# Optimization experiments

Measured on AMD Instinct MI355X. Metric: run time of the kernel, lower is better.

The kernel has to match this reference:

```python
import jax, jax.numpy as jnp
import numpy as np

# Static config (matches init_kwargs)
B, T_IN, H, W, C_IN = 32, 12, 64, 64, 4
T_OUT, C_OUT = 12, 4
K, S = 8, 4            # unfold kernel and stride (stride = K // 2); H%K==0 -> padding 0
DEC_K = 25             # series decomposition moving-average window
O = T_OUT * C_OUT      # number of per-output locally-connected filters
NH = (H - K) // S + 1  # 15
NW = (W - K) // S + 1  # 15
L = NH * NW            # 225 patches


def setup_inputs() -> dict:
    key = jax.random.key(0)
    k1, k2, k3 = jax.random.split(key, 3)
    x = jax.random.normal(k1, (B, T_IN, H, W, C_IN), jnp.float32)
    # torch init: weights ~ randn, biases zeros; stacked over the O = C_out*T_out loop
    w_s = jax.random.normal(k2, (O, T_IN, C_IN, K, K), jnp.float32)
    w_t = jax.random.normal(k3, (O, T_IN, C_IN, K, K), jnp.float32)
    b_s = jnp.zeros((O, K, K), jnp.float32)
    b_t = jnp.zeros((O, K, K), jnp.float32)
    return {"x": x, "w_s": w_s, "b_s": b_s, "w_t": w_t, "b_t": b_t}


def _moving_avg(x):
    # x: (B, T, N). Replicate-pad time by (DEC_K-1)//2 on each side, mean over DEC_K window.
    p = (DEC_K - 1) // 2
    xp = jnp.concatenate([jnp.repeat(x[:, :1], p, axis=1), x,
                          jnp.repeat(x[:, -1:], p, axis=1)], axis=1)
    cs = jnp.concatenate([jnp.zeros_like(xp[:, :1]), jnp.cumsum(xp, axis=1)], axis=1)
    return (cs[:, DEC_K:] - cs[:, :-DEC_K]) / DEC_K  # (B, T, N)


def _patch_idx():
    ii = (jnp.arange(NH) * S)[:, None] + jnp.arange(K)  # (NH, K)
    jj = (jnp.arange(NW) * S)[:, None] + jnp.arange(K)  # (NW, K)
    return ii, jj


def _unfold(x):
    # x: (B, Cc, H, W) -> patches (B, L, Cc, K, K), L row-major over (NH, NW) as in nn.Unfold
    ii, jj = _patch_idx()
    p = x[:, :, ii]              # (B, Cc, NH, K, W)
    p = p[:, :, :, :, jj]        # (B, Cc, NH, K, NW, K)
    p = p.transpose(0, 2, 4, 1, 3, 5)  # (B, NH, NW, Cc, K, K)
    return p.reshape(x.shape[0], L, x.shape[1], K, K)


def _fold(p):
    # p: (B, Cc, L, K, K) -> (B, Cc, H, W), summing overlapping contributions (nn.Fold)
    Bb, Cc = p.shape[0], p.shape[1]
    p = p.reshape(Bb, Cc, NH, NW, K, K).transpose(0, 1, 2, 4, 3, 5)  # (B,Cc,NH,K,NW,K)
    ii, jj = _patch_idx()
    I = ii[:, :, None, None]     # (NH, K, 1, 1)
    J = jj[None, None, :, :]     # (1, 1, NW, K)
    out = jnp.zeros((Bb, Cc, H, W), p.dtype)
    return out.at[:, :, I, J].add(p)


def reference(x, w_s, b_s, w_t, b_t):
    # (B, T, H, W, C) -> (B, T, C*H*W), decompose along time
    xf = x.transpose(0, 1, 4, 2, 3).reshape(B, T_IN, -1)
    trend = _moving_avg(xf)
    res = xf - trend
    out = jnp.zeros((B, L, O, K, K), x.dtype)
    for comp, w, b in ((res, w_s, b_s), (trend, w_t, b_t)):
        xc = comp.reshape(B, T_IN * C_IN, H, W)
        patches = _unfold(xc).reshape(B, L, T_IN, C_IN, K, K)
        # locally-connected linear: per (i,j) position, contract over (T_in, C_in) into O outputs
        out = out + jnp.einsum('bltcij,otcij->bloij', patches, w) + b
    out = out.transpose(0, 2, 1, 3, 4)            # (B, O, L, K, K)
    out = _fold(out)                              # (B, O, H, W)
    out = out.reshape(B, T_OUT, C_OUT, H, W).transpose(0, 1, 3, 4, 2)
    return out                                    # (B, T_out, H, W, C_out)
```

## Files before the change

kernel.cpp:

```cpp
#include <hip/hip_runtime.h>


typedef _Float16 h2 __attribute__((ext_vector_type(2)));
typedef _Float16 f16x8 __attribute__((ext_vector_type(8)));
typedef float f32x4 __attribute__((ext_vector_type(4)));
union F4F16 { float4 f4; f16x8 h8; };

__global__ __launch_bounds__(64) void pack_weights(const float* __restrict__ w_s,
                                                   const float* __restrict__ b_s,
                                                   const float* __restrict__ w_t,
                                                   const float* __restrict__ b_t,
                                                   float* __restrict__ PW) {
    int o = blockIdx.x;
    int s = threadIdx.x;
    float* dst = PW + (size_t)(s * 48 + o) * 64;
    float w0[4] = {0.f, 0.f, 0.f, 0.f};
    float w1[4] = {0.f, 0.f, 0.f, 0.f};
#pragma unroll
    for (int t = 0; t < 12; ++t) {
#pragma unroll
        for (int c = 0; c < 4; ++c) {
            int wi = ((o * 12 + t) * 4 + c) * 64 + s;
            float ws = w_s[wi];
            float wt = w_t[wi];
            dst[t * 4 + c] = ws;
            float d = wt - ws;
            w0[c] += d;
            w1[c] += (float)t * d;
        }
    }
#pragma unroll
    for (int c = 0; c < 4; ++c) {
        dst[48 + c] = w0[c];
        dst[52 + c] = w1[c];
    }
    dst[56] = b_s[o * 64 + s] + b_t[o * 64 + s];
#pragma unroll
    for (int k = 57; k < 64; ++k) dst[k] = 0.f;
}

__global__ __launch_bounds__(64) void pack_frags(const float* __restrict__ PW,
                                                 float4* __restrict__ PWF) {
    int blk = blockIdx.x;
    int cls = blk / 12;
    int to = blk % 12;
    int L = threadIdx.x;
    int n16 = L & 15, quad = L >> 4;
    int c = n16 >> 2, r = n16 & 3;
    int o = to * 4 + c;
    int rh = cls >> 2, rw = cls & 3;
    int s = (rh + 4 * (r >> 1)) * 8 + (rw + 4 * (r & 1));
    const float* src = PW + (size_t)(s * 48 + o) * 64;
#pragma unroll
    for (int ks = 0; ks < 2; ++ks) {
        F4F16 u;
#pragma unroll
        for (int j = 0; j < 8; ++j) {
            int k = ks * 32 + quad * 8 + j;
            u.h8[j] = (_Float16)src[k];
        }
        PWF[((size_t)blk * 2 + ks) * 64 + L] = u.f4;
    }
}

__global__ __launch_bounds__(256, 2) void dlinear_mfma(const float* __restrict__ x,
                                                       const float4* __restrict__ PWF,
                                                       float* __restrict__ out) {
    __shared__ float4 As[256 * 9];
    int tid = threadIdx.x;
    int wv = tid >> 6, L = tid & 63;
    int cls = blockIdx.x & 15;
    int bb = blockIdx.x >> 4;
    int rh = cls >> 2, rw = cls & 3;

    f16x8 bf[12][2];
#pragma unroll
    for (int to = 0; to < 12; ++to)
#pragma unroll
        for (int ks = 0; ks < 2; ++ks) {
            F4F16 u;
            u.f4 = PWF[((size_t)(cls * 12 + to) * 2 + ks) * 64 + L];
            bf[to][ks] = u.h8;
        }

    int hh = tid >> 4, ww = tid & 15;
    int h = 4 * hh + rh, wcol0 = 4 * ww + rw;
    const float4* xb = (const float4*)x + (size_t)bb * 12 * 4096 + h * 64 + wcol0;

    h2 X2[32] __attribute__((aligned(16)));
    {
        float sx = 0.f, sy = 0.f, sz = 0.f, sw = 0.f;
        float4 first, last;
#pragma unroll
        for (int t = 0; t < 12; ++t) {
            float4 v = xb[t * 4096];
            if (t == 0) first = v;
            if (t == 11) last = v;
            h2 a, b;
            a[0] = (_Float16)v.x; a[1] = (_Float16)v.y;
            b[0] = (_Float16)v.z; b[1] = (_Float16)v.w;
            X2[2 * t] = a;
            X2[2 * t + 1] = b;
            sx += v.x; sy += v.y; sz += v.z; sw += v.w;
        }
        const float inv25 = 1.f / 25.f;
        float A0 = (sx + 12.f * first.x + last.x) * inv25;
        float A1 = (sy + 12.f * first.y + last.y) * inv25;
        float A2 = (sz + 12.f * first.z + last.z) * inv25;
        float A3 = (sw + 12.f * first.w + last.w) * inv25;
        float D0 = (last.x - first.x) * inv25;
        float D1 = (last.y - first.y) * inv25;
        float D2 = (last.z - first.z) * inv25;
        float D3 = (last.w - first.w) * inv25;
        h2 t0, t1, t2, t3, t4, z;
        t0[0] = (_Float16)A0; t0[1] = (_Float16)A1;
        t1[0] = (_Float16)A2; t1[1] = (_Float16)A3;
        t2[0] = (_Float16)D0; t2[1] = (_Float16)D1;
        t3[0] = (_Float16)D2; t3[1] = (_Float16)D3;
        t4[0] = (_Float16)1.f; t4[1] = (_Float16)0.f;
        z[0] = (_Float16)0.f; z[1] = (_Float16)0.f;
        X2[24] = t0; X2[25] = t1; X2[26] = t2; X2[27] = t3;
        X2[28] = t4; X2[29] = z; X2[30] = z; X2[31] = z;
    }
#pragma unroll
    for (int j = 0; j < 8; ++j) As[tid * 9 + j] = ((float4*)X2)[j];
    __syncthreads();

    int quad = L >> 4, mlane = L & 15;
    f16x8 af[4][2];
#pragma unroll
    for (int mt = 0; mt < 4; ++mt) {
        int p = wv * 64 + mt * 16 + mlane;
#pragma unroll
        for (int ks = 0; ks < 2; ++ks) {
            F4F16 u;
            u.f4 = As[p * 9 + ks * 4 + quad];
            af[mt][ks] = u.h8;
        }
    }

    int r = L & 3, cch = (L >> 2) & 3;
    bool dj = (r & 1) != 0;
    bool di = (r & 2) != 0;
    float* outb = out + (size_t)bb * 12 * 16384;

#pragma unroll
    for (int to = 0; to < 12; ++to) {
#pragma unroll
        for (int mt = 0; mt < 4; ++mt) {
            f32x4 d = {0.f, 0.f, 0.f, 0.f};
            d = __builtin_amdgcn_mfma_f32_16x16x32_f16(af[mt][0], bf[to][0], d, 0, 0, 0);
            d = __builtin_amdgcn_mfma_f32_16x16x32_f16(af[mt][1], bf[to][1], d, 0, 0, 0);
            int hq = wv * 4 + mt;
            bool okh = di ? (hq >= 1) : (hq <= 14);
            float s_[4];
#pragma unroll
            for (int reg = 0; reg < 4; ++reg) {
                int mm = quad * 4 + reg;
                bool okw = dj ? (mm >= 1) : (mm <= 14);
                float v = (okh && okw) ? d[reg] : 0.f;
                v += __shfl_xor(v, 1);
                v += __shfl_xor(v, 2);
                s_[reg] = v;
            }
            float val = (r == 0) ? s_[0] : (r == 1) ? s_[1] : (r == 2) ? s_[2] : s_[3];
            int wc = 16 * quad + 4 * r + rw;
            outb[(size_t)to * 16384 + (4 * hq + rh) * 256 + wc * 4 + cch] = val;
        }
    }
}

extern "C" void kernel_launch(void* const* d_in, const int* in_sizes, int n_in,
                              void* d_out, int out_size, void* d_ws, size_t ws_size,
                              hipStream_t stream) {
    const float* x = (const float*)d_in[0];
    const float* w_s = (const float*)d_in[1];
    const float* b_s = (const float*)d_in[2];
    const float* w_t = (const float*)d_in[3];
    const float* b_t = (const float*)d_in[4];
    float* out = (float*)d_out;
    float* PW = (float*)d_ws;
    float4* PWF = (float4*)((char*)d_ws + 48 * 64 * 64 * 4);

    pack_weights<<<48, 64, 0, stream>>>(w_s, b_s, w_t, b_t, PW);
    pack_frags<<<192, 64, 0, stream>>>(PW, PWF);
    dlinear_mfma<<<32 * 16, 256, 0, stream>>>(x, PWF, out);
}
```

Baseline: 111.6 us.

## Swap MFMA operands to reduce patch sums in-lane and store float4 outputs

Puts the weights in the MFMA A operand and the patches in B, so each lane holds the four fold-offset rows for one channel and can sum them without cross-lane shuffles. Per-wave LDS staging then gathers the four channels per pixel, giving coalesced float4 global stores instead of scalar stores. The two weight-packing kernels are also merged into one, removing a launch and an intermediate buffer. The cost is extra LDS traffic per output tile, and the cross-iteration reuse of the LDS buffer depends on in-order LDS operations within a wave.

```diff
diff --git a/kernel.cpp b/kernel.cpp
--- a/kernel.cpp
+++ b/kernel.cpp
@@ -6,58 +6,46 @@
 typedef float f32x4 __attribute__((ext_vector_type(4)));
 union F4F16 { float4 f4; f16x8 h8; };
 
-__global__ __launch_bounds__(64) void pack_weights(const float* __restrict__ w_s,
-                                                   const float* __restrict__ b_s,
-                                                   const float* __restrict__ w_t,
-                                                   const float* __restrict__ b_t,
-                                                   float* __restrict__ PW) {
-    int o = blockIdx.x;
-    int s = threadIdx.x;
-    float* dst = PW + (size_t)(s * 48 + o) * 64;
-    float w0[4] = {0.f, 0.f, 0.f, 0.f};
-    float w1[4] = {0.f, 0.f, 0.f, 0.f};
-#pragma unroll
-    for (int t = 0; t < 12; ++t) {
-#pragma unroll
-        for (int c = 0; c < 4; ++c) {
-            int wi = ((o * 12 + t) * 4 + c) * 64 + s;
-            float ws = w_s[wi];
-            float wt = w_t[wi];
-            dst[t * 4 + c] = ws;
-            float d = wt - ws;
-            w0[c] += d;
-            w1[c] += (float)t * d;
-        }
-    }
-#pragma unroll
-    for (int c = 0; c < 4; ++c) {
-        dst[48 + c] = w0[c];
-        dst[52 + c] = w1[c];
-    }
-    dst[56] = b_s[o * 64 + s] + b_t[o * 64 + s];
-#pragma unroll
-    for (int k = 57; k < 64; ++k) dst[k] = 0.f;
-}
-
-__global__ __launch_bounds__(64) void pack_frags(const float* __restrict__ PW,
+__global__ __launch_bounds__(64) void pack_frags(const float* __restrict__ w_s,
+                                                 const float* __restrict__ b_s,
+                                                 const float* __restrict__ w_t,
+                                                 const float* __restrict__ b_t,
                                                  float4* __restrict__ PWF) {
     int blk = blockIdx.x;
     int cls = blk / 12;
     int to = blk % 12;
     int L = threadIdx.x;
-    int n16 = L & 15, quad = L >> 4;
-    int c = n16 >> 2, r = n16 & 3;
+    int m16 = L & 15, quad = L >> 4;
+    int c = m16 >> 2, r = m16 & 3;
     int o = to * 4 + c;
     int rh = cls >> 2, rw = cls & 3;
     int s = (rh + 4 * (r >> 1)) * 8 + (rw + 4 * (r & 1));
-    const float* src = PW + (size_t)(s * 48 + o) * 64;
+    const float* Wsb = w_s + (size_t)o * 3072 + s;
+    const float* Wtb = w_t + (size_t)o * 3072 + s;
 #pragma unroll
     for (int ks = 0; ks < 2; ++ks) {
         F4F16 u;
 #pragma unroll
         for (int j = 0; j < 8; ++j) {
             int k = ks * 32 + quad * 8 + j;
-            u.h8[j] = (_Float16)src[k];
+            float val;
+            if (k < 48) {
+                val = Wsb[k * 64];
+            } else if (k < 56) {
+                int c2 = k & 3;
+                bool isW1 = (k & 4) != 0;
+                float acc = 0.f;
+                for (int t = 0; t < 12; ++t) {
+                    float d = Wtb[(t * 4 + c2) * 64] - Wsb[(t * 4 + c2) * 64];
+                    acc += isW1 ? (float)t * d : d;
+                }
+                val = acc;
+            } else if (k == 56) {
+                val = b_s[o * 64 + s] + b_t[o * 64 + s];
+            } else {
+                val = 0.f;
+            }
+            u.h8[j] = (_Float16)val;
         }
         PWF[((size_t)blk * 2 + ks) * 64 + L] = u.f4;
     }
@@ -67,24 +55,25 @@
                                                        const float4* __restrict__ PWF,
                                                        float* __restrict__ out) {
     __shared__ float4 As[256 * 9];
+    __shared__ __align__(16) float Es[4][256];
     int tid = threadIdx.x;
     int wv = tid >> 6, L = tid & 63;
     int cls = blockIdx.x & 15;
     int bb = blockIdx.x >> 4;
     int rh = cls >> 2, rw = cls & 3;
 
-    f16x8 bf[12][2];
+    f16x8 wf[12][2];
 #pragma unroll
     for (int to = 0; to < 12; ++to)
 #pragma unroll
         for (int ks = 0; ks < 2; ++ks) {
             F4F16 u;
             u.f4 = PWF[((size_t)(cls * 12 + to) * 2 + ks) * 64 + L];
-            bf[to][ks] = u.h8;
+            wf[to][ks] = u.h8;
         }
 
-    int hh = tid >> 4, ww = tid & 15;
-    int h = 4 * hh + rh, wcol0 = 4 * ww + rw;
+    int hh = tid >> 4, wwp = tid & 15;
+    int h = 4 * hh + rh, wcol0 = 4 * wwp + rw;
     const float4* xb = (const float4*)x + (size_t)bb * 12 * 4096 + h * 64 + wcol0;
 
     h2 X2[32] __attribute__((aligned(16)));
@@ -126,47 +115,42 @@
     for (int j = 0; j < 8; ++j) As[tid * 9 + j] = ((float4*)X2)[j];
     __syncthreads();
 
-    int quad = L >> 4, mlane = L & 15;
-    f16x8 af[4][2];
+    int quad = L >> 4, nlane = L & 15;
+    f16x8 pf[4][2];
 #pragma unroll
-    for (int mt = 0; mt < 4; ++mt) {
-        int p = wv * 64 + mt * 16 + mlane;
+    for (int g = 0; g < 4; ++g) {
+        int p = wv * 64 + g * 16 + nlane;
 #pragma unroll
         for (int ks = 0; ks < 2; ++ks) {
             F4F16 u;
             u.f4 = As[p * 9 + ks * 4 + quad];
-            af[mt][ks] = u.h8;
+            pf[g][ks] = u.h8;
         }
     }
 
-    int r = L & 3, cch = (L >> 2) & 3;
-    bool dj = (r & 1) != 0;
-    bool di = (r & 2) != 0;
-    float* outb = out + (size_t)bb * 12 * 16384;
+    bool okw0 = nlane <= 14, okw1 = nlane >= 1;
+    float4* ob = (float4*)out + (size_t)bb * 12 * 4096;
+    int rdpix = wv * 64 + L;
+    int st_hh = rdpix >> 4, st_ww = rdpix & 15;
+    float4* stp = ob + (4 * st_hh + rh) * 64 + (4 * st_ww + rw);
 
 #pragma unroll
     for (int to = 0; to < 12; ++to) {
 #pragma unroll
-        for (int mt = 0; mt < 4; ++mt) {
+        for (int g = 0; g < 4; ++g) {
             f32x4 d = {0.f, 0.f, 0.f, 0.f};
-            d = __builtin_amdgcn_mfma_f32_16x16x32_f16(af[mt][0], bf[to][0], d, 0, 0, 0);
-            d = __builtin_amdgcn_mfma_f32_16x16x32_f16(af[mt][1], bf[to][1], d, 0, 0, 0);
-            int hq = wv * 4 + mt;
-            bool okh = di ? (hq >= 1) : (hq <= 14);
-            float s_[4];
-#pragma unroll
-            for (int reg = 0; reg < 4; ++reg) {
-                int mm = quad * 4 + reg;
-                bool okw = dj ? (mm >= 1) : (mm <= 14);
-                float v = (okh && okw) ? d[reg] : 0.f;
-                v += __shfl_xor(v, 1);
-                v += __shfl_xor(v, 2);
-                s_[reg] = v;
-            }
-            float val = (r == 0) ? s_[0] : (r == 1) ? s_[1] : (r == 2) ? s_[2] : s_[3];
-            int wc = 16 * quad + 4 * r + rw;
-            outb[(size_t)to * 16384 + (4 * hq + rh) * 256 + wc * 4 + cch] = val;
+            d = __builtin_amdgcn_mfma_f32_16x16x32_f16(wf[to][0], pf[g][0], d, 0, 0, 0);
+            d = __builtin_amdgcn_mfma_f32_16x16x32_f16(wf[to][1], pf[g][1], d, 0, 0, 0);
+            int hq = wv * 4 + g;
+            bool okh0 = hq <= 14, okh1 = hq >= 1;
+            float v = ((okh0 && okw0) ? d[0] : 0.f)
+                    + ((okh0 && okw1) ? d[1] : 0.f)
+                    + ((okh1 && okw0) ? d[2] : 0.f)
+                    + ((okh1 && okw1) ? d[3] : 0.f);
+            Es[wv][g * 64 + nlane * 4 + quad] = v;
         }
+        float4 r = *(const float4*)&Es[wv][4 * L];
+        stp[to * 4096] = r;
     }
 }
 
@@ -179,10 +163,8 @@
     const float* w_t = (const float*)d_in[3];
     const float* b_t = (const float*)d_in[4];
     float* out = (float*)d_out;
-    float* PW = (float*)d_ws;
-    float4* PWF = (float4*)((char*)d_ws + 48 * 64 * 64 * 4);
+    float4* PWF = (float4*)d_ws;
 
-    pack_weights<<<48, 64, 0, stream>>>(w_s, b_s, w_t, b_t, PW);
-    pack_frags<<<192, 64, 0, stream>>>(PW, PWF);
+    pack_frags<<<192, 64, 0, stream>>>(w_s, b_s, w_t, b_t, PWF);
     dlinear_mfma<<<32 * 16, 256, 0, stream>>>(x, PWF, out);
 }
```

Measured after the change: 112.7 us. Within noise of the previous version (+0.9%).
